# Kernel tuning notes

Hardware: AMD Instinct MI355X
Metric: run time of the kernel (lower is better)

The kernel has to match this reference:

```python
import jax, jax.numpy as jnp
import numpy as np

BLOCK = 256  # query block size for banded computation
NEG = -1e30


def _sliding_window_attention(q, k, v, window_size, block=BLOCK):
    # q, k, v: [B, H, S, D]; mask: |q_idx - kv_idx| <= window_size
    B, H, S, D = q.shape
    w = int(window_size)
    nb = S // block
    Wk = block + 2 * w  # keys visible to one query block
    scale = D ** -0.5

    # pad keys/values by w on each side so every block sees a fixed-size window
    k_pad = jnp.pad(k, ((0, 0), (0, 0), (w, w), (0, 0)))
    v_pad = jnp.pad(v, ((0, 0), (0, 0), (w, w), (0, 0)))

    # padded key indices for each query block: [nb, Wk]
    idx = (jnp.arange(nb) * block)[:, None] + jnp.arange(Wk)[None, :]
    k_win = k_pad[:, :, idx, :]  # [B, H, nb, Wk, D]
    v_win = v_pad[:, :, idx, :]
    qb = q.reshape(B, H, nb, block, D)

    # banded scores: never materialize the full S x S matrix
    scores = jnp.einsum('bhncd,bhnwd->bhncw', qb, k_win) * scale

    a = jnp.arange(block)[:, None]   # query offset within block
    b = jnp.arange(Wk)[None, :]      # key offset within window
    band = (b - a >= 0) & (b - a <= 2 * w)           # |q - kv| <= w
    kv_global = idx - w                               # [nb, Wk]
    valid = (kv_global >= 0) & (kv_global < S)        # exclude padding
    mask = band[None, :, :] & valid[:, None, :]       # [nb, block, Wk]

    scores = jnp.where(mask[None, None], scores, NEG)
    probs = jax.nn.softmax(scores, axis=-1)
    out = jnp.einsum('bhncw,bhnwd->bhncd', probs, v_win)
    return out.reshape(B, H, S, D)


def setup_inputs() -> dict:
    key = jax.random.key(0)
    kq, kk, kv = jax.random.split(key, 3)
    B, H, S, D = 1, 16, 8192, 64
    return {
        'query': jax.random.normal(kq, (B, H, S, D), dtype=jnp.float32),
        'key': jax.random.normal(kk, (B, H, S, D), dtype=jnp.float32),
        'value': jax.random.normal(kv, (B, H, S, D), dtype=jnp.float32),
        'batch_size': 1,
        'window_size': 256,
    }


def reference(query, key, value, batch_size, window_size):
    # batch_size is unused in the original math (signature compatibility only)
    return _sliding_window_attention(query, key, value, window_size)
```

## Files before the change

### kernel.cpp

```cpp
#include <hip/hip_runtime.h>
#include <hip/hip_bf16.h>


#define NH  16
#define SEQ 8192
#define HD  64
#define QT  256
#define NW  8
#define KVB 64
#define NEGV -1e30f
#define NTILE (SEQ / KVB)
#define TILE_ELEMS (KVB * HD)

typedef __bf16 bf16x8 __attribute__((ext_vector_type(8)));
typedef float  f32x4  __attribute__((ext_vector_type(4)));

__device__ __forceinline__ int prow_of(int key) {
    return ((key >> 2) & 1) * 32 + ((key >> 5) & 1) * 16
         + ((key >> 3) & 3) * 4  + (key & 3);
}

__global__ __launch_bounds__(512) void prepack(
    const float* __restrict__ K, const float* __restrict__ V,
    __bf16* __restrict__ kpp, __bf16* __restrict__ vpp)
{
    const int b   = blockIdx.x;
    const int isV = b >= NH * NTILE;
    const int t   = isV ? b - NH * NTILE : b;
    const int tid = threadIdx.x;

    const float* src = (isV ? V : K) + (size_t)t * TILE_ELEMS;
    __bf16*      dst = (isV ? vpp : kpp) + (size_t)t * TILE_ELEMS;

    if (!isV) {
        const int key = tid >> 3, c = tid & 7;
        const float* s = src + key * HD + c * 8;
        float4 a = *(const float4*)s;
        float4 q = *(const float4*)(s + 4);
        bf16x8 o;
        o[0]=(__bf16)a.x; o[1]=(__bf16)a.y; o[2]=(__bf16)a.z; o[3]=(__bf16)a.w;
        o[4]=(__bf16)q.x; o[5]=(__bf16)q.y; o[6]=(__bf16)q.z; o[7]=(__bf16)q.w;
        const int pr = prow_of(key);
        *(bf16x8*)&dst[pr * 64 + ((c * 8) ^ ((pr & 7) << 3))] = o;
    } else {
        __shared__ float Vl[64][65];
        const int key = tid >> 3, c = tid & 7;
        const float* s = src + key * HD + c * 8;
        float4 a = *(const float4*)s;
        float4 q = *(const float4*)(s + 4);
        Vl[key][c*8+0]=a.x; Vl[key][c*8+1]=a.y; Vl[key][c*8+2]=a.z; Vl[key][c*8+3]=a.w;
        Vl[key][c*8+4]=q.x; Vl[key][c*8+5]=q.y; Vl[key][c*8+6]=q.z; Vl[key][c*8+7]=q.w;
        __syncthreads();
        const int vd = tid >> 3, kc = tid & 7;
        bf16x8 o;
#pragma unroll
        for (int j = 0; j < 8; ++j) o[j] = (__bf16)Vl[kc*8 + j][vd];
        *(bf16x8*)&dst[vd * 64 + ((kc * 8) ^ ((vd & 7) << 3))] = o;
    }
}

#define GLOAD_LDS16(G, L)                                                      \
    __builtin_amdgcn_global_load_lds(                                          \
        (const __attribute__((address_space(1))) void*)(G),                    \
        (__attribute__((address_space(3))) void*)(L), 16, 0, 0)

__global__ __launch_bounds__(512) void swa_fwd(
    const float* __restrict__ Q, const __bf16* __restrict__ kpp,
    const __bf16* __restrict__ vpp, float* __restrict__ O,
    const int* __restrict__ wsz)
{
    const int w    = wsz[0];
    const int w2   = 2 * w;

    const int lin = blockIdx.x;
    const int xcd = lin & 7;
    const int i2  = lin >> 3;
    const int h   = 2 * xcd + (i2 >> 5);
    const int q0  = (i2 & 31) * QT;

    const int tid  = threadIdx.x;
    const int lane = tid & 63;
    const int wv   = tid >> 6;
    const int l15  = lane & 15;
    const int g    = lane >> 4;

    const float* Qh = Q + (size_t)h * SEQ * HD;
    float*       Oh = O + (size_t)h * SEQ * HD;

    __shared__ __align__(16) __bf16 Ks[2][TILE_ELEMS];
    __shared__ __align__(16) __bf16 Vt[2][TILE_ELEMS];

    const float qscale = 0.125f * 1.44269504f;
    bf16x8 qf[2][2];
#pragma unroll
    for (int rb = 0; rb < 2; ++rb)
#pragma unroll
        for (int ks = 0; ks < 2; ++ks) {
            const float* src = Qh + (size_t)(q0 + wv*32 + rb*16 + l15) * HD + ks*32 + g*8;
            float4 a = *(const float4*)src;
            float4 b = *(const float4*)(src + 4);
            bf16x8 t;
            t[0] = (__bf16)(a.x * qscale); t[1] = (__bf16)(a.y * qscale);
            t[2] = (__bf16)(a.z * qscale); t[3] = (__bf16)(a.w * qscale);
            t[4] = (__bf16)(b.x * qscale); t[5] = (__bf16)(b.y * qscale);
            t[6] = (__bf16)(b.z * qscale); t[7] = (__bf16)(b.w * qscale);
            qf[rb][ks] = t;
        }

    f32x4 acc[2][4];
    float lrp[2] = {0.f, 0.f};
#pragma unroll
    for (int rb = 0; rb < 2; ++rb)
#pragma unroll
        for (int db = 0; db < 4; ++db)
            acc[rb][db] = f32x4{0.f, 0.f, 0.f, 0.f};

    int kv_lo = q0 - w; if (kv_lo < 0) kv_lo = 0; kv_lo &= ~(KVB - 1);
    int kv_hi = q0 + QT + w; if (kv_hi > SEQ) kv_hi = SEQ;
    kv_hi = (kv_hi + KVB - 1) & ~(KVB - 1);
    const int nT = (kv_hi - kv_lo) / KVB;

    const int rw0 = q0 + wv * 32;

    const size_t headTileBase = (size_t)h * NTILE * TILE_ELEMS;
    const int    chunkOff     = wv * 512 + lane * 8;

#define STAGE_TILE(TI, BUF)                                                    \
    {                                                                          \
        const size_t tb = headTileBase + (size_t)(TI) * TILE_ELEMS;            \
        GLOAD_LDS16(kpp + tb + chunkOff, &Ks[BUF][wv * 512]);                  \
        GLOAD_LDS16(vpp + tb + chunkOff, &Vt[BUF][wv * 512]);                  \
    }

#define WG_BARRIER()                                                           \
    asm volatile("s_waitcnt vmcnt(0) lgkmcnt(0)" ::: "memory");                \
    __builtin_amdgcn_sched_barrier(0);                                         \
    __builtin_amdgcn_s_barrier();                                              \
    __builtin_amdgcn_sched_barrier(0);

    STAGE_TILE(kv_lo >> 6, 0);
    WG_BARRIER();

    for (int it = 0; it < nT; ++it) {
        const int kb = kv_lo + it * KVB;
        const __bf16* Kb = &Ks[it & 1][0];
        const __bf16* Vb = &Vt[it & 1][0];

        if (it + 1 < nT) STAGE_TILE((kb >> 6) + 1, (it + 1) & 1);

        if (kb <= rw0 + 31 + w && kb + KVB - 1 >= rw0 - w) {
            const int sw = (l15 & 7) << 3;

            f32x4 st[2][4];
#pragma unroll
            for (int t = 0; t < 4; ++t) {
                bf16x8 kf0 = *(const bf16x8*)&Kb[(t*16 + l15)*64 + ((     g*8) ^ sw)];
                bf16x8 kf1 = *(const bf16x8*)&Kb[(t*16 + l15)*64 + ((32 + g*8) ^ sw)];
                f32x4 z0{0.f,0.f,0.f,0.f}, z1{0.f,0.f,0.f,0.f};
                z0       = __builtin_amdgcn_mfma_f32_16x16x32_bf16(kf0, qf[0][0], z0, 0,0,0);
                st[0][t] = __builtin_amdgcn_mfma_f32_16x16x32_bf16(kf1, qf[0][1], z0, 0,0,0);
                z1       = __builtin_amdgcn_mfma_f32_16x16x32_bf16(kf0, qf[1][0], z1, 0,0,0);
                st[1][t] = __builtin_amdgcn_mfma_f32_16x16x32_bf16(kf1, qf[1][1], z1, 0,0,0);
            }

            const bool full = (kb + KVB-1 - rw0 <= w) && (kb - (rw0 + 31) >= -w);
            if (!full) {
#pragma unroll
                for (int rb = 0; rb < 2; ++rb) {
                    const int relb = kb + g*8 + w - (rw0 + rb*16) - l15;
#pragma unroll
                    for (int t = 0; t < 4; ++t)
#pragma unroll
                        for (int r = 0; r < 4; ++r)
                            if ((unsigned)(relb + (t&1)*32 + (t>>1)*4 + r) > (unsigned)w2)
                                st[rb][t][r] = NEGV;
                }
            }

            float p[2][4][4];
#pragma unroll
            for (int rb = 0; rb < 2; ++rb) {
#pragma unroll
                for (int t = 0; t < 4; ++t)
#pragma unroll
                    for (int r = 0; r < 4; ++r)
                        p[rb][t][r] = __builtin_amdgcn_exp2f(fminf(st[rb][t][r], 80.f));
                float s01 = (p[rb][0][0] + p[rb][0][1]) + (p[rb][0][2] + p[rb][0][3]);
                float s23 = (p[rb][1][0] + p[rb][1][1]) + (p[rb][1][2] + p[rb][1][3]);
                float s45 = (p[rb][2][0] + p[rb][2][1]) + (p[rb][2][2] + p[rb][2][3]);
                float s67 = (p[rb][3][0] + p[rb][3][1]) + (p[rb][3][2] + p[rb][3][3]);
                lrp[rb] += (s01 + s23) + (s45 + s67);
            }

#pragma unroll
            for (int kh = 0; kh < 2; ++kh) {
                bf16x8 pf0, pf1;
                pf0[0]=(__bf16)p[0][kh][0];   pf0[1]=(__bf16)p[0][kh][1];
                pf0[2]=(__bf16)p[0][kh][2];   pf0[3]=(__bf16)p[0][kh][3];
                pf0[4]=(__bf16)p[0][kh+2][0]; pf0[5]=(__bf16)p[0][kh+2][1];
                pf0[6]=(__bf16)p[0][kh+2][2]; pf0[7]=(__bf16)p[0][kh+2][3];
                pf1[0]=(__bf16)p[1][kh][0];   pf1[1]=(__bf16)p[1][kh][1];
                pf1[2]=(__bf16)p[1][kh][2];   pf1[3]=(__bf16)p[1][kh][3];
                pf1[4]=(__bf16)p[1][kh+2][0]; pf1[5]=(__bf16)p[1][kh+2][1];
                pf1[6]=(__bf16)p[1][kh+2][2]; pf1[7]=(__bf16)p[1][kh+2][3];
#pragma unroll
                for (int db = 0; db < 4; ++db) {
                    bf16x8 vfr = *(const bf16x8*)&Vb[(db*16 + l15)*64 + ((kh*32 + g*8) ^ sw)];
                    acc[0][db] = __builtin_amdgcn_mfma_f32_16x16x32_bf16(pf0, vfr, acc[0][db], 0,0,0);
                    acc[1][db] = __builtin_amdgcn_mfma_f32_16x16x32_bf16(pf1, vfr, acc[1][db], 0,0,0);
                }
            }
        }

        WG_BARRIER();
    }

#pragma unroll
    for (int rb = 0; rb < 2; ++rb) {
        float lr = lrp[rb];
        lr += __shfl_xor(lr, 16);
        lr += __shfl_xor(lr, 32);
        const float il = 1.0f / lr;
        float inv[4];
#pragma unroll
        for (int r = 0; r < 4; ++r) inv[r] = __shfl(il, g*4 + r);
#pragma unroll
        for (int db = 0; db < 4; ++db)
#pragma unroll
            for (int r = 0; r < 4; ++r) {
                const int row = rw0 + rb*16 + g*4 + r;
                Oh[(size_t)row * HD + db*16 + l15] = acc[rb][db][r] * inv[r];
            }
    }
}

__global__ __launch_bounds__(512) void swa_fwd_fb(
    const float* __restrict__ Q, const float* __restrict__ K,
    const float* __restrict__ V, float* __restrict__ O,
    const int* __restrict__ wsz)
{
    const int w    = wsz[0];
    const int w2   = 2 * w;
    const int lin = blockIdx.x;
    const int xcd = lin & 7;
    const int i2  = lin >> 3;
    const int h   = 2 * xcd + (i2 >> 6);
    const int q0  = (i2 & 63) * 128;
    const int tid  = threadIdx.x;
    const int lane = tid & 63;
    const int wv   = tid >> 6;
    const int l15  = lane & 15;
    const int g    = lane >> 4;
    const size_t hoff = (size_t)h * SEQ * HD;
    const float* Qh = Q + hoff;
    const float* Kh = K + hoff;
    const float* Vh = V + hoff;
    float*       Oh = O + hoff;
    __shared__ __align__(16) __bf16 Ks[2][KVB * 64];
    __shared__ __align__(16) __bf16 Vt[2][64 * 64];
    const float qscale = 0.125f * 1.44269504f;
    const int   qrow   = q0 + wv * 16 + l15;
    bf16x8 qf[2];
#pragma unroll
    for (int ks = 0; ks < 2; ++ks) {
        const float* src = Qh + (size_t)qrow * HD + ks*32 + g*8;
        float4 a = *(const float4*)src;
        float4 b = *(const float4*)(src + 4);
        bf16x8 t;
        t[0] = (__bf16)(a.x * qscale); t[1] = (__bf16)(a.y * qscale);
        t[2] = (__bf16)(a.z * qscale); t[3] = (__bf16)(a.w * qscale);
        t[4] = (__bf16)(b.x * qscale); t[5] = (__bf16)(b.y * qscale);
        t[6] = (__bf16)(b.z * qscale); t[7] = (__bf16)(b.w * qscale);
        qf[ks] = t;
    }
    f32x4 acc[4];
    float lrp = 0.f;
#pragma unroll
    for (int db = 0; db < 4; ++db) acc[db] = f32x4{0.f, 0.f, 0.f, 0.f};
    int kv_lo = q0 - w; if (kv_lo < 0) kv_lo = 0; kv_lo &= ~(KVB - 1);
    int kv_hi = q0 + 128 + w; if (kv_hi > SEQ) kv_hi = SEQ;
    kv_hi = (kv_hi + KVB - 1) & ~(KVB - 1);
    const int nT = (kv_hi - kv_lo) / KVB;
    const int rw0 = q0 + wv * 16;
    const int kkey = tid >> 3, kd8 = (tid & 7) * 8;
    const int prow = prow_of(kkey);
    const int swk  = (prow & 7) << 3;
    const int vd   = tid & 63, vk0 = (tid >> 6) * 8;
    const int swv  = (vd & 7) << 3;
    float4 kpa, kpb;
    float  vp[8];
#define ISSUE_LOADS_FB(KB)                                                     \
    {                                                                          \
        const float* ksrc = Kh + (size_t)((KB) + kkey) * HD + kd8;             \
        kpa = *(const float4*)ksrc;                                            \
        kpb = *(const float4*)(ksrc + 4);                                      \
        const float* vsrc = Vh + (size_t)((KB) + vk0) * HD + vd;               \
        _Pragma("unroll")                                                      \
        for (int j = 0; j < 8; ++j) vp[j] = vsrc[j * HD];                      \
    }
#define CVT_STORE_FB(BUF)                                                      \
    {                                                                          \
        bf16x8 tk;                                                             \
        tk[0] = (__bf16)kpa.x; tk[1] = (__bf16)kpa.y;                          \
        tk[2] = (__bf16)kpa.z; tk[3] = (__bf16)kpa.w;                          \
        tk[4] = (__bf16)kpb.x; tk[5] = (__bf16)kpb.y;                          \
        tk[6] = (__bf16)kpb.z; tk[7] = (__bf16)kpb.w;                          \
        *(bf16x8*)&Ks[BUF][prow*64 + (kd8 ^ swk)] = tk;                        \
        bf16x8 tv;                                                             \
        _Pragma("unroll")                                                      \
        for (int j = 0; j < 8; ++j) tv[j] = (__bf16)vp[j];                     \
        *(bf16x8*)&Vt[BUF][vd*64 + (vk0 ^ swv)] = tv;                          \
    }
#define WG_BARRIER_FB()                                                        \
    asm volatile("s_waitcnt lgkmcnt(0)" ::: "memory");                         \
    __builtin_amdgcn_sched_barrier(0);                                         \
    __builtin_amdgcn_s_barrier();                                              \
    __builtin_amdgcn_sched_barrier(0);
    ISSUE_LOADS_FB(kv_lo);
    CVT_STORE_FB(0);
    if (nT > 1) ISSUE_LOADS_FB(kv_lo + KVB);
    WG_BARRIER_FB();
    for (int it = 0; it < nT; ++it) {
        const int kb = kv_lo + it * KVB;
        const __bf16* Kb = &Ks[it & 1][0];
        const __bf16* Vb = &Vt[it & 1][0];
        if (kb <= rw0 + 15 + w && kb + KVB - 1 >= rw0 - w) {
            const int sw = (l15 & 7) << 3;
            f32x4 st[4];
#pragma unroll
            for (int t = 0; t < 4; ++t) {
                bf16x8 kf0 = *(const bf16x8*)&Kb[(t*16 + l15)*64 + ((     g*8) ^ sw)];
                bf16x8 kf1 = *(const bf16x8*)&Kb[(t*16 + l15)*64 + ((32 + g*8) ^ sw)];
                f32x4 z{0.f, 0.f, 0.f, 0.f};
                z     = __builtin_amdgcn_mfma_f32_16x16x32_bf16(kf0, qf[0], z, 0,0,0);
                st[t] = __builtin_amdgcn_mfma_f32_16x16x32_bf16(kf1, qf[1], z, 0,0,0);
            }
            const bool full = (kb + KVB-1 - rw0 <= w) && (kb - (rw0 + 15) >= -w);
            if (!full) {
                const int relb = kb + g*8 + w - rw0 - l15;
#pragma unroll
                for (int t = 0; t < 4; ++t)
#pragma unroll
                    for (int r = 0; r < 4; ++r)
                        if ((unsigned)(relb + (t&1)*32 + (t>>1)*4 + r) > (unsigned)w2)
                            st[t][r] = NEGV;
            }
            float p[4][4];
#pragma unroll
            for (int t = 0; t < 4; ++t)
#pragma unroll
                for (int r = 0; r < 4; ++r)
                    p[t][r] = __builtin_amdgcn_exp2f(fminf(st[t][r], 80.f));
            float s01 = (p[0][0] + p[0][1]) + (p[0][2] + p[0][3]);
            float s23 = (p[1][0] + p[1][1]) + (p[1][2] + p[1][3]);
            float s45 = (p[2][0] + p[2][1]) + (p[2][2] + p[2][3]);
            float s67 = (p[3][0] + p[3][1]) + (p[3][2] + p[3][3]);
            lrp += (s01 + s23) + (s45 + s67);
#pragma unroll
            for (int kh = 0; kh < 2; ++kh) {
                bf16x8 pf;
                pf[0] = (__bf16)p[kh][0];   pf[1] = (__bf16)p[kh][1];
                pf[2] = (__bf16)p[kh][2];   pf[3] = (__bf16)p[kh][3];
                pf[4] = (__bf16)p[kh+2][0]; pf[5] = (__bf16)p[kh+2][1];
                pf[6] = (__bf16)p[kh+2][2]; pf[7] = (__bf16)p[kh+2][3];
#pragma unroll
                for (int db = 0; db < 4; ++db) {
                    bf16x8 vfr = *(const bf16x8*)&Vb[(db*16 + l15)*64 + ((kh*32 + g*8) ^ sw)];
                    acc[db] = __builtin_amdgcn_mfma_f32_16x16x32_bf16(pf, vfr, acc[db], 0,0,0);
                }
            }
        }
        if (it + 1 < nT) {
            CVT_STORE_FB((it + 1) & 1);
            if (it + 2 < nT) ISSUE_LOADS_FB(kb + 2 * KVB);
        }
        WG_BARRIER_FB();
    }
    float lr = lrp;
    lr += __shfl_xor(lr, 16);
    lr += __shfl_xor(lr, 32);
    const float il = 1.0f / lr;
    float inv[4];
#pragma unroll
    for (int r = 0; r < 4; ++r) inv[r] = __shfl(il, g*4 + r);
#pragma unroll
    for (int db = 0; db < 4; ++db)
#pragma unroll
        for (int r = 0; r < 4; ++r) {
            const int row = rw0 + g*4 + r;
            Oh[(size_t)row * HD + db*16 + l15] = acc[db][r] * inv[r];
        }
}

extern "C" void kernel_launch(void* const* d_in, const int* in_sizes, int n_in,
                              void* d_out, int out_size, void* d_ws, size_t ws_size,
                              hipStream_t stream) {
    const float* Q   = (const float*)d_in[0];
    const float* K   = (const float*)d_in[1];
    const float* V   = (const float*)d_in[2];
    const int*   wsz = (const int*)d_in[4];
    float* O = (float*)d_out;

    const size_t imgBytes = (size_t)NH * NTILE * TILE_ELEMS * sizeof(__bf16);
    if (ws_size >= 2 * imgBytes) {
        __bf16* kpp = (__bf16*)d_ws;
        __bf16* vpp = (__bf16*)((char*)d_ws + imgBytes);
        prepack<<<dim3(2 * NH * NTILE), dim3(512), 0, stream>>>(K, V, kpp, vpp);
        swa_fwd<<<dim3((SEQ / QT) * NH), dim3(512), 0, stream>>>(Q, kpp, vpp, O, wsz);
    } else {
        swa_fwd_fb<<<dim3((SEQ / 128) * NH), dim3(512), 0, stream>>>(Q, K, V, O, wsz);
    }
}
```

Before: 56.65 us.

## Load prepacked K/V fragments directly into registers per wave, dropping LDS staging

Prepack now writes K and V tiles in the exact per-lane MFMA fragment order, so each wave loads its fragments from global memory as coalesced uint4 reads into registers. The shared-memory double buffer and workgroup barriers are removed, and each wave iterates only over its own KV range. The next K tile is register-prefetched. In exchange, the waves of a workgroup no longer share staged tiles, so global/L2 traffic rises and register pressure grows with the 24 uint4 buffers.

```diff
diff --git a/kernel.cpp b/kernel.cpp
--- a/kernel.cpp
+++ b/kernel.cpp
@@ -11,14 +11,10 @@
 #define NEGV -1e30f
 #define NTILE (SEQ / KVB)
 #define TILE_ELEMS (KVB * HD)
+#define TILE_U4    (TILE_ELEMS / 8)
 
 typedef __bf16 bf16x8 __attribute__((ext_vector_type(8)));
 typedef float  f32x4  __attribute__((ext_vector_type(4)));
-
-__device__ __forceinline__ int prow_of(int key) {
-    return ((key >> 2) & 1) * 32 + ((key >> 5) & 1) * 16
-         + ((key >> 3) & 3) * 4  + (key & 3);
-}
 
 __global__ __launch_bounds__(512) void prepack(
     const float* __restrict__ K, const float* __restrict__ V,
@@ -26,51 +22,48 @@
 {
     const int b   = blockIdx.x;
     const int isV = b >= NH * NTILE;
-    const int t   = isV ? b - NH * NTILE : b;
+    const int t0  = isV ? b - NH * NTILE : b;
     const int tid = threadIdx.x;
 
-    const float* src = (isV ? V : K) + (size_t)t * TILE_ELEMS;
-    __bf16*      dst = (isV ? vpp : kpp) + (size_t)t * TILE_ELEMS;
-
-    if (!isV) {
+    const float* src = (isV ? V : K) + (size_t)t0 * TILE_ELEMS;
+    __bf16*      dst = (isV ? vpp : kpp) + (size_t)t0 * TILE_ELEMS;
+
+    __shared__ float Tl[64][65];
+    {
         const int key = tid >> 3, c = tid & 7;
         const float* s = src + key * HD + c * 8;
         float4 a = *(const float4*)s;
         float4 q = *(const float4*)(s + 4);
-        bf16x8 o;
-        o[0]=(__bf16)a.x; o[1]=(__bf16)a.y; o[2]=(__bf16)a.z; o[3]=(__bf16)a.w;
-        o[4]=(__bf16)q.x; o[5]=(__bf16)q.y; o[6]=(__bf16)q.z; o[7]=(__bf16)q.w;
-        const int pr = prow_of(key);
-        *(bf16x8*)&dst[pr * 64 + ((c * 8) ^ ((pr & 7) << 3))] = o;
+        Tl[key][c*8+0]=a.x; Tl[key][c*8+1]=a.y; Tl[key][c*8+2]=a.z; Tl[key][c*8+3]=a.w;
+        Tl[key][c*8+4]=q.x; Tl[key][c*8+5]=q.y; Tl[key][c*8+6]=q.z; Tl[key][c*8+7]=q.w;
+    }
+    __syncthreads();
+
+    const int f = tid >> 6, l = tid & 63, i = l & 15, gg = l >> 4;
+    bf16x8 o;
+    if (!isV) {
+        const int t = f >> 1, ks = f & 1;
+        const int kk = (t & 1) * 32 + (i >> 2) * 8 + (t >> 1) * 4 + (i & 3);
+        const int d0 = ks * 32 + gg * 8;
+#pragma unroll
+        for (int j = 0; j < 8; ++j) o[j] = (__bf16)Tl[kk][d0 + j];
     } else {
-        __shared__ float Vl[64][65];
-        const int key = tid >> 3, c = tid & 7;
-        const float* s = src + key * HD + c * 8;
-        float4 a = *(const float4*)s;
-        float4 q = *(const float4*)(s + 4);
-        Vl[key][c*8+0]=a.x; Vl[key][c*8+1]=a.y; Vl[key][c*8+2]=a.z; Vl[key][c*8+3]=a.w;
-        Vl[key][c*8+4]=q.x; Vl[key][c*8+5]=q.y; Vl[key][c*8+6]=q.z; Vl[key][c*8+7]=q.w;
-        __syncthreads();
-        const int vd = tid >> 3, kc = tid & 7;
-        bf16x8 o;
-#pragma unroll
-        for (int j = 0; j < 8; ++j) o[j] = (__bf16)Vl[kc*8 + j][vd];
-        *(bf16x8*)&dst[vd * 64 + ((kc * 8) ^ ((vd & 7) << 3))] = o;
-    }
-}
-
-#define GLOAD_LDS16(G, L)                                                      \
-    __builtin_amdgcn_global_load_lds(                                          \
-        (const __attribute__((address_space(1))) void*)(G),                    \
-        (__attribute__((address_space(3))) void*)(L), 16, 0, 0)
+        const int kh = f >> 2, db = f & 3;
+        const int d  = db * 16 + i;
+        const int k0 = kh * 32 + gg * 8;
+#pragma unroll
+        for (int j = 0; j < 8; ++j) o[j] = (__bf16)Tl[k0 + j][d];
+    }
+    *(bf16x8*)&dst[tid * 8] = o;
+}
 
 __global__ __launch_bounds__(512) void swa_fwd(
     const float* __restrict__ Q, const __bf16* __restrict__ kpp,
     const __bf16* __restrict__ vpp, float* __restrict__ O,
     const int* __restrict__ wsz)
 {
-    const int w    = wsz[0];
-    const int w2   = 2 * w;
+    const int w  = wsz[0];
+    const int w2 = 2 * w;
 
     const int lin = blockIdx.x;
     const int xcd = lin & 7;
@@ -86,9 +79,6 @@
 
     const float* Qh = Q + (size_t)h * SEQ * HD;
     float*       Oh = O + (size_t)h * SEQ * HD;
-
-    __shared__ __align__(16) __bf16 Ks[2][TILE_ELEMS];
-    __shared__ __align__(16) __bf16 Vt[2][TILE_ELEMS];
 
     const float qscale = 0.125f * 1.44269504f;
     bf16x8 qf[2][2];
@@ -115,104 +105,93 @@
         for (int db = 0; db < 4; ++db)
             acc[rb][db] = f32x4{0.f, 0.f, 0.f, 0.f};
 
-    int kv_lo = q0 - w; if (kv_lo < 0) kv_lo = 0; kv_lo &= ~(KVB - 1);
-    int kv_hi = q0 + QT + w; if (kv_hi > SEQ) kv_hi = SEQ;
+    const int rw0 = q0 + wv * 32;
+    int kv_lo = rw0 - w; if (kv_lo < 0) kv_lo = 0; kv_lo &= ~(KVB - 1);
+    int kv_hi = rw0 + 32 + w; if (kv_hi > SEQ) kv_hi = SEQ;
     kv_hi = (kv_hi + KVB - 1) & ~(KVB - 1);
     const int nT = (kv_hi - kv_lo) / KVB;
 
-    const int rw0 = q0 + wv * 32;
-
-    const size_t headTileBase = (size_t)h * NTILE * TILE_ELEMS;
-    const int    chunkOff     = wv * 512 + lane * 8;
-
-#define STAGE_TILE(TI, BUF)                                                    \
-    {                                                                          \
-        const size_t tb = headTileBase + (size_t)(TI) * TILE_ELEMS;            \
-        GLOAD_LDS16(kpp + tb + chunkOff, &Ks[BUF][wv * 512]);                  \
-        GLOAD_LDS16(vpp + tb + chunkOff, &Vt[BUF][wv * 512]);                  \
-    }
-
-#define WG_BARRIER()                                                           \
-    asm volatile("s_waitcnt vmcnt(0) lgkmcnt(0)" ::: "memory");                \
-    __builtin_amdgcn_sched_barrier(0);                                         \
-    __builtin_amdgcn_s_barrier();                                              \
-    __builtin_amdgcn_sched_barrier(0);
-
-    STAGE_TILE(kv_lo >> 6, 0);
-    WG_BARRIER();
+    const size_t tb0 = ((size_t)h * NTILE + (kv_lo >> 6)) * TILE_U4;
+    const uint4* kt = (const uint4*)kpp + tb0;
+    const uint4* vt = (const uint4*)vpp + tb0;
+
+    uint4 kC[8], kN[8], vC[8];
+#pragma unroll
+    for (int f = 0; f < 8; ++f) kC[f] = kt[f * 64 + lane];
 
     for (int it = 0; it < nT; ++it) {
         const int kb = kv_lo + it * KVB;
-        const __bf16* Kb = &Ks[it & 1][0];
-        const __bf16* Vb = &Vt[it & 1][0];
-
-        if (it + 1 < nT) STAGE_TILE((kb >> 6) + 1, (it + 1) & 1);
-
-        if (kb <= rw0 + 31 + w && kb + KVB - 1 >= rw0 - w) {
-            const int sw = (l15 & 7) << 3;
-
-            f32x4 st[2][4];
-#pragma unroll
-            for (int t = 0; t < 4; ++t) {
-                bf16x8 kf0 = *(const bf16x8*)&Kb[(t*16 + l15)*64 + ((     g*8) ^ sw)];
-                bf16x8 kf1 = *(const bf16x8*)&Kb[(t*16 + l15)*64 + ((32 + g*8) ^ sw)];
-                f32x4 z0{0.f,0.f,0.f,0.f}, z1{0.f,0.f,0.f,0.f};
-                z0       = __builtin_amdgcn_mfma_f32_16x16x32_bf16(kf0, qf[0][0], z0, 0,0,0);
-                st[0][t] = __builtin_amdgcn_mfma_f32_16x16x32_bf16(kf1, qf[0][1], z0, 0,0,0);
-                z1       = __builtin_amdgcn_mfma_f32_16x16x32_bf16(kf0, qf[1][0], z1, 0,0,0);
-                st[1][t] = __builtin_amdgcn_mfma_f32_16x16x32_bf16(kf1, qf[1][1], z1, 0,0,0);
-            }
-
-            const bool full = (kb + KVB-1 - rw0 <= w) && (kb - (rw0 + 31) >= -w);
-            if (!full) {
-#pragma unroll
-                for (int rb = 0; rb < 2; ++rb) {
-                    const int relb = kb + g*8 + w - (rw0 + rb*16) - l15;
-#pragma unroll
-                    for (int t = 0; t < 4; ++t)
-#pragma unroll
-                        for (int r = 0; r < 4; ++r)
-                            if ((unsigned)(relb + (t&1)*32 + (t>>1)*4 + r) > (unsigned)w2)
-                                st[rb][t][r] = NEGV;
-                }
-            }
-
-            float p[2][4][4];
+
+        const uint4* vtp = vt + (size_t)it * TILE_U4;
+#pragma unroll
+        for (int f = 0; f < 8; ++f) vC[f] = vtp[f * 64 + lane];
+        const int itn = (it + 1 < nT) ? (it + 1) : it;
+        const uint4* ktn = kt + (size_t)itn * TILE_U4;
+#pragma unroll
+        for (int f = 0; f < 8; ++f) kN[f] = ktn[f * 64 + lane];
+
+        f32x4 st[2][4];
+#pragma unroll
+        for (int t = 0; t < 4; ++t) {
+            bf16x8 kf0 = __builtin_bit_cast(bf16x8, kC[t*2]);
+            bf16x8 kf1 = __builtin_bit_cast(bf16x8, kC[t*2+1]);
+            f32x4 z0{0.f,0.f,0.f,0.f}, z1{0.f,0.f,0.f,0.f};
+            z0       = __builtin_amdgcn_mfma_f32_16x16x32_bf16(kf0, qf[0][0], z0, 0,0,0);
+            st[0][t] = __builtin_amdgcn_mfma_f32_16x16x32_bf16(kf1, qf[0][1], z0, 0,0,0);
+            z1       = __builtin_amdgcn_mfma_f32_16x16x32_bf16(kf0, qf[1][0], z1, 0,0,0);
+            st[1][t] = __builtin_amdgcn_mfma_f32_16x16x32_bf16(kf1, qf[1][1], z1, 0,0,0);
+        }
+
+        const bool full = (kb + KVB-1 - rw0 <= w) && (kb - (rw0 + 31) >= -w);
+        if (!full) {
 #pragma unroll
             for (int rb = 0; rb < 2; ++rb) {
+                const int relb = kb + g*8 + w - (rw0 + rb*16) - l15;
 #pragma unroll
                 for (int t = 0; t < 4; ++t)
 #pragma unroll
                     for (int r = 0; r < 4; ++r)
-                        p[rb][t][r] = __builtin_amdgcn_exp2f(fminf(st[rb][t][r], 80.f));
-                float s01 = (p[rb][0][0] + p[rb][0][1]) + (p[rb][0][2] + p[rb][0][3]);
-                float s23 = (p[rb][1][0] + p[rb][1][1]) + (p[rb][1][2] + p[rb][1][3]);
-                float s45 = (p[rb][2][0] + p[rb][2][1]) + (p[rb][2][2] + p[rb][2][3]);
-                float s67 = (p[rb][3][0] + p[rb][3][1]) + (p[rb][3][2] + p[rb][3][3]);
-                lrp[rb] += (s01 + s23) + (s45 + s67);
-            }
-
-#pragma unroll
-            for (int kh = 0; kh < 2; ++kh) {
-                bf16x8 pf0, pf1;
-                pf0[0]=(__bf16)p[0][kh][0];   pf0[1]=(__bf16)p[0][kh][1];
-                pf0[2]=(__bf16)p[0][kh][2];   pf0[3]=(__bf16)p[0][kh][3];
-                pf0[4]=(__bf16)p[0][kh+2][0]; pf0[5]=(__bf16)p[0][kh+2][1];
-                pf0[6]=(__bf16)p[0][kh+2][2]; pf0[7]=(__bf16)p[0][kh+2][3];
-                pf1[0]=(__bf16)p[1][kh][0];   pf1[1]=(__bf16)p[1][kh][1];
-                pf1[2]=(__bf16)p[1][kh][2];   pf1[3]=(__bf16)p[1][kh][3];
-                pf1[4]=(__bf16)p[1][kh+2][0]; pf1[5]=(__bf16)p[1][kh+2][1];
-                pf1[6]=(__bf16)p[1][kh+2][2]; pf1[7]=(__bf16)p[1][kh+2][3];
-#pragma unroll
-                for (int db = 0; db < 4; ++db) {
-                    bf16x8 vfr = *(const bf16x8*)&Vb[(db*16 + l15)*64 + ((kh*32 + g*8) ^ sw)];
-                    acc[0][db] = __builtin_amdgcn_mfma_f32_16x16x32_bf16(pf0, vfr, acc[0][db], 0,0,0);
-                    acc[1][db] = __builtin_amdgcn_mfma_f32_16x16x32_bf16(pf1, vfr, acc[1][db], 0,0,0);
-                }
-            }
-        }
-
-        WG_BARRIER();
+                        if ((unsigned)(relb + (t&1)*32 + (t>>1)*4 + r) > (unsigned)w2)
+                            st[rb][t][r] = NEGV;
+            }
+        }
+
+        float p[2][4][4];
+#pragma unroll
+        for (int rb = 0; rb < 2; ++rb) {
+#pragma unroll
+            for (int t = 0; t < 4; ++t)
+#pragma unroll
+                for (int r = 0; r < 4; ++r)
+                    p[rb][t][r] = __builtin_amdgcn_exp2f(fminf(st[rb][t][r], 80.f));
+            float s01 = (p[rb][0][0] + p[rb][0][1]) + (p[rb][0][2] + p[rb][0][3]);
+            float s23 = (p[rb][1][0] + p[rb][1][1]) + (p[rb][1][2] + p[rb][1][3]);
+            float s45 = (p[rb][2][0] + p[rb][2][1]) + (p[rb][2][2] + p[rb][2][3]);
+            float s67 = (p[rb][3][0] + p[rb][3][1]) + (p[rb][3][2] + p[rb][3][3]);
+            lrp[rb] += (s01 + s23) + (s45 + s67);
+        }
+
+#pragma unroll
+        for (int kh = 0; kh < 2; ++kh) {
+            bf16x8 pf0, pf1;
+            pf0[0]=(__bf16)p[0][kh][0];   pf0[1]=(__bf16)p[0][kh][1];
+            pf0[2]=(__bf16)p[0][kh][2];   pf0[3]=(__bf16)p[0][kh][3];
+            pf0[4]=(__bf16)p[0][kh+2][0]; pf0[5]=(__bf16)p[0][kh+2][1];
+            pf0[6]=(__bf16)p[0][kh+2][2]; pf0[7]=(__bf16)p[0][kh+2][3];
+            pf1[0]=(__bf16)p[1][kh][0];   pf1[1]=(__bf16)p[1][kh][1];
+            pf1[2]=(__bf16)p[1][kh][2];   pf1[3]=(__bf16)p[1][kh][3];
+            pf1[4]=(__bf16)p[1][kh+2][0]; pf1[5]=(__bf16)p[1][kh+2][1];
+            pf1[6]=(__bf16)p[1][kh+2][2]; pf1[7]=(__bf16)p[1][kh+2][3];
+#pragma unroll
+            for (int db = 0; db < 4; ++db) {
+                bf16x8 vfr = __builtin_bit_cast(bf16x8, vC[kh*4 + db]);
+                acc[0][db] = __builtin_amdgcn_mfma_f32_16x16x32_bf16(pf0, vfr, acc[0][db], 0,0,0);
+                acc[1][db] = __builtin_amdgcn_mfma_f32_16x16x32_bf16(pf1, vfr, acc[1][db], 0,0,0);
+            }
+        }
+
+#pragma unroll
+        for (int f = 0; f < 8; ++f) kC[f] = kN[f];
     }
 
 #pragma unroll
@@ -234,6 +213,10 @@
     }
 }
 
+__device__ __forceinline__ int prow_of(int key) {
+    return ((key >> 2) & 1) * 32 + ((key >> 5) & 1) * 16
+         + ((key >> 3) & 3) * 4  + (key & 3);
+}
 __global__ __launch_bounds__(512) void swa_fwd_fb(
     const float* __restrict__ Q, const float* __restrict__ K,
     const float* __restrict__ V, float* __restrict__ O,
```

New measurement: 55.95 us. About the same (-1.2%).
